# Performance work log

Hardware: AMD Instinct MI355X
Metric: run time of the kernel (lower is better)

Reference implementation:

```python
import jax, jax.numpy as jnp
import numpy as np

B, L, A, K = 8, 256, 15, 9
EDGE_SIZE = 16
CA = 1  # BBHeavyAtom.CA index


def setup_inputs() -> dict:
    key = jax.random.key(0)
    k1, k2, k3, k4 = jax.random.split(key, 4)
    pos_heavyatom = jax.random.normal(k1, (B, L, A, 3), jnp.float32) * 3.0
    aa = jax.random.randint(k2, (B, L), 0, 21, jnp.int32)
    atom_types = jax.random.randint(k3, (B, L, A), 0, 38, jnp.int32)
    mask_atoms = jnp.ones((B, L, A), dtype=bool)
    block_lengths = jnp.full((B, L), A, jnp.int32)
    lengths = jnp.full((B,), L, jnp.int32)
    # two segments per sample (e.g. antibody / antigen) so intra+inter edges exist
    fragment_type = jnp.broadcast_to((jnp.arange(L) >= L // 2).astype(jnp.int32), (B, L))
    edge_emb = jax.random.normal(k4, (2, EDGE_SIZE), jnp.float32) * 0.02
    return {"pos_heavyatom": pos_heavyatom, "aa": aa, "atom_types": atom_types,
            "mask_atoms": mask_atoms, "block_lengths": block_lengths,
            "lengths": lengths, "fragment_type": fragment_type, "edge_emb": edge_emb}


def _block_dist(pos, mask_atoms):
    """Min unit-pair distance between every pair of blocks. pos [B,L,A,3] -> [B,L,L]."""
    Xf = pos.reshape(B, L * A, 3)
    x2 = jnp.sum(Xf * Xf, axis=-1)  # [B, N]
    d2 = x2[:, :, None] + x2[:, None, :] - 2.0 * jnp.einsum('bnd,bmd->bnm', Xf, Xf)
    d = jnp.sqrt(jnp.maximum(d2, 0.0))  # [B, N, N]
    # unit is kept iff its atom mask AND its residue's CA mask are set
    mask_res = mask_atoms[:, :, CA]                           # [B, L]
    valid = (mask_atoms & mask_res[:, :, None]).reshape(B, L * A)
    pair_ok = valid[:, :, None] & valid[:, None, :]
    d = jnp.where(pair_ok, d, jnp.inf)
    # scatter_min over block edges == min over the (A, A) unit-pair tiles
    return d.reshape(B, L, A, L, A).min(axis=(2, 4))          # [B, L, L]


def _knn_edges(dist, cand_mask):
    """For each source block (row), pick K nearest candidate dst blocks. Returns [2, B*L*K] global ids."""
    dm = jnp.where(cand_mask, dist, jnp.inf)
    _, idx = jax.lax.top_k(-dm, K)                            # [B, L, K] local dst ids
    src = jnp.broadcast_to(jnp.arange(L, dtype=jnp.int32)[None, :, None], (B, L, K))
    offs = (jnp.arange(B, dtype=jnp.int32) * L)[:, None, None]
    return jnp.stack([(src + offs).reshape(-1), (idx.astype(jnp.int32) + offs).reshape(-1)], axis=0)


def reference(pos_heavyatom, aa, atom_types, mask_atoms, block_lengths, lengths,
              fragment_type, edge_emb):
    # segment ids: fragment_type 2 is merged into segment 1
    seg = jnp.where(fragment_type == 2, 1, fragment_type)     # [B, L]
    dist = _block_dist(pos_heavyatom, mask_atoms)             # [B, L, L]

    same_seg = seg[:, :, None] == seg[:, None, :]
    eye = jnp.eye(L, dtype=bool)[None]
    intra_edges = _knn_edges(dist, same_seg & ~eye)           # same segment, no self-loop
    inter_edges = _knn_edges(dist, ~same_seg)                 # different segment

    edges = jnp.concatenate([intra_edges, inter_edges], axis=1)  # [2, 2*B*L*K]
    edge_type = jnp.concatenate([jnp.zeros(intra_edges.shape[1], jnp.int32),
                                 jnp.ones(inter_edges.shape[1], jnp.int32)])
    edge_attr = edge_emb[edge_type]                           # [2*B*L*K, 16]

    block_id = jnp.arange(B * L * A, dtype=jnp.int32) // A    # global block id per unit
    batch_id = jnp.arange(B * L, dtype=jnp.int32) // L        # batch id per block
    return block_id, batch_id, edges, edge_attr
```

## Files before the change

### kernel.cpp

```cpp
#include <hip/hip_runtime.h>


#define BB   8
#define LL   256
#define AA   15
#define KK   9

#define O_EDGES   32768
#define NE_HALF   18432
#define NE        36864
#define O_ATTR    106496
#define N_ATTR    589824

__global__ __launch_bounds__(256) void dist_knn_kernel(
    const float* __restrict__ pos,
    const int*   __restrict__ frag,
    float*       __restrict__ out)
{
    const int b = blockIdx.x / LL;
    const int i = blockIdx.x % LL;
    const int j = threadIdx.x;

    __shared__ double dAi[AA * 3];
    __shared__ double dX2i[AA];
    __shared__ double sDist[LL];
    __shared__ int    sSeg[LL];

    if (j < AA * 3) dAi[j] = (double)pos[(size_t)(b * LL + i) * (AA * 3) + j];
    __syncthreads();
    if (j < AA) {
        double x0 = dAi[j * 3 + 0], x1 = dAi[j * 3 + 1], x2 = dAi[j * 3 + 2];
        dX2i[j] = x0 * x0 + x1 * x1 + x2 * x2;
    }

    double xj[AA][3];
    double x2j[AA];
    const float* pj = pos + (size_t)(b * LL + j) * (AA * 3);
    #pragma unroll
    for (int c = 0; c < AA; ++c) {
        xj[c][0] = (double)pj[c * 3 + 0];
        xj[c][1] = (double)pj[c * 3 + 1];
        xj[c][2] = (double)pj[c * 3 + 2];
        x2j[c] = xj[c][0] * xj[c][0] + xj[c][1] * xj[c][1] + xj[c][2] * xj[c][2];
    }
    int ft  = frag[b * LL + j];
    int seg = (ft == 2) ? 1 : ft;
    __syncthreads();

    double d2min = INFINITY;
    for (int a = 0; a < AA; ++a) {
        double a0 = dAi[a * 3 + 0], a1 = dAi[a * 3 + 1], a2 = dAi[a * 3 + 2];
        double x2a = dX2i[a];
        #pragma unroll
        for (int c = 0; c < AA; ++c) {
            double dot = a0 * xj[c][0] + a1 * xj[c][1] + a2 * xj[c][2];
            double d2  = (x2a + x2j[c]) - 2.0 * dot;
            d2min = fmin(d2min, d2);
        }
    }
    sDist[j] = fmax(d2min, 0.0);
    sSeg[j]  = seg;
    __syncthreads();

    if (j < 64) {
        const int seg_i = sSeg[i];
        const int row   = b * LL + i;
        for (int pass = 0; pass < 2; ++pass) {
            double dl[4];
            int    il[4];
            #pragma unroll
            for (int q = 0; q < 4; ++q) {
                int cand = j + q * 64;
                int sc   = sSeg[cand];
                bool ok  = (pass == 0) ? (sc == seg_i && cand != i)
                                       : (sc != seg_i);
                dl[q] = ok ? sDist[cand] : INFINITY;
                il[q] = cand;
            }
            for (int k = 0; k < KK; ++k) {
                double v = dl[0]; int id = il[0];
                #pragma unroll
                for (int q = 1; q < 4; ++q)
                    if (dl[q] < v || (dl[q] == v && il[q] < id)) { v = dl[q]; id = il[q]; }
                for (int off = 1; off < 64; off <<= 1) {
                    double ov = __shfl_xor(v, off, 64);
                    int    oi = __shfl_xor(id, off, 64);
                    if (ov < v || (ov == v && oi < id)) { v = ov; id = oi; }
                }
                if ((id & 63) == j) dl[id >> 6] = INFINITY;
                if (j == 0) {
                    int e = (pass == 0 ? 0 : NE_HALF) + row * KK + k;
                    out[O_EDGES + e]      = (float)row;
                    out[O_EDGES + NE + e] = (float)(b * LL + id);
                }
            }
        }
    }
}

__global__ __launch_bounds__(256) void fill_kernel(
    const float* __restrict__ emb,
    float*       __restrict__ out)
{
    __shared__ float semb[32];
    if (threadIdx.x < 32) semb[threadIdx.x] = emb[threadIdx.x];
    __syncthreads();

    int t = blockIdx.x * blockDim.x + threadIdx.x;
    if (t < 30720) out[t] = (float)(t / AA);
    if (t < 2048)  out[30720 + t] = (float)(t >> 8);
    if (t < N_ATTR) {
        int row = t >> 4;
        int col = t & 15;
        out[O_ATTR + t] = semb[(row < NE_HALF ? 0 : 16) + col];
    }
}

extern "C" void kernel_launch(void* const* d_in, const int* in_sizes, int n_in,
                              void* d_out, int out_size, void* d_ws, size_t ws_size,
                              hipStream_t stream) {
    const float* pos  = (const float*)d_in[0];
    const int*   frag = (const int*)d_in[6];
    const float* emb  = (const float*)d_in[7];
    float* out = (float*)d_out;

    dist_knn_kernel<<<dim3(BB * LL), dim3(256), 0, stream>>>(pos, frag, out);
    fill_kernel<<<dim3((N_ATTR + 255) / 256), dim3(256), 0, stream>>>(emb, out);
}
```

Before: 111.2 us.

## Screen distances in fp32, refine candidates in fp64, fuse fill kernel

The all-pairs min-distance pass now runs in fp32 with split min accumulators. Each row's 9th-nearest value per pass sets a threshold, and only candidates within a small margin of it have their distances recomputed in fp64. The final top-k selection then runs on those refined values, so ties and near-ties still resolve as before. The separate fill kernel for block_id, batch_id and edge_attr is folded into the same kernel, which removes a launch. The fixed DELTA margin risks missing a true neighbour if fp32 error exceeds it, and the refinement adds extra syncs and global reads.

```diff
diff --git a/kernel.cpp b/kernel.cpp
--- a/kernel.cpp
+++ b/kernel.cpp
@@ -6,75 +6,165 @@
 #define AA   15
 #define KK   9
 
+#define O_BATCH   30720
 #define O_EDGES   32768
 #define NE_HALF   18432
 #define NE        36864
 #define O_ATTR    106496
 #define N_ATTR    589824
-
-__global__ __launch_bounds__(256) void dist_knn_kernel(
+#define DELTA     0.02f
+
+__global__ __launch_bounds__(256) void edge_fused_kernel(
     const float* __restrict__ pos,
     const int*   __restrict__ frag,
+    const float* __restrict__ emb,
     float*       __restrict__ out)
 {
-    const int b = blockIdx.x / LL;
-    const int i = blockIdx.x % LL;
-    const int j = threadIdx.x;
-
-    __shared__ double dAi[AA * 3];
-    __shared__ double dX2i[AA];
-    __shared__ double sDist[LL];
+    const int blk = blockIdx.x;
+    const int b   = blk >> 8;
+    const int i   = blk & 255;
+    const int j   = threadIdx.x;
+
+    __shared__ float  sAi[45];
+    __shared__ float  sX2i[AA];
+    __shared__ float  sD32[LL];
     __shared__ int    sSeg[LL];
-
-    if (j < AA * 3) dAi[j] = (double)pos[(size_t)(b * LL + i) * (AA * 3) + j];
+    __shared__ double sD64[LL];
+    __shared__ int    sList[LL];
+    __shared__ int    sCnt;
+    __shared__ float  sV9[2];
+
+    if (j < AA)  out[blk * AA + j]  = (float)blk;
+    if (j == AA) out[O_BATCH + blk] = (float)b;
+    {
+        int idx = blk * 288 + j;
+        int e = idx >> 4, col = idx & 15;
+        out[O_ATTR + idx] = emb[(e < NE_HALF ? 0 : 16) + col];
+        if (j < 32) {
+            int idx2 = idx + 256;
+            int e2 = idx2 >> 4, col2 = idx2 & 15;
+            out[O_ATTR + idx2] = emb[(e2 < NE_HALF ? 0 : 16) + col2];
+        }
+    }
+
+    if (j < 45)  sAi[j] = pos[(size_t)blk * 45 + j];
+    if (j == 255) sCnt = 0;
+    sD64[j] = INFINITY;
     __syncthreads();
     if (j < AA) {
-        double x0 = dAi[j * 3 + 0], x1 = dAi[j * 3 + 1], x2 = dAi[j * 3 + 2];
-        dX2i[j] = x0 * x0 + x1 * x1 + x2 * x2;
-    }
-
-    double xj[AA][3];
-    double x2j[AA];
-    const float* pj = pos + (size_t)(b * LL + j) * (AA * 3);
+        float x0 = sAi[3*j], x1 = sAi[3*j+1], x2 = sAi[3*j+2];
+        sX2i[j] = x0*x0 + x1*x1 + x2*x2;
+    }
+
+    float xj[AA][3], x2j[AA];
+    const float* pj = pos + (size_t)(b * LL + j) * 45;
     #pragma unroll
     for (int c = 0; c < AA; ++c) {
-        xj[c][0] = (double)pj[c * 3 + 0];
-        xj[c][1] = (double)pj[c * 3 + 1];
-        xj[c][2] = (double)pj[c * 3 + 2];
-        x2j[c] = xj[c][0] * xj[c][0] + xj[c][1] * xj[c][1] + xj[c][2] * xj[c][2];
-    }
-    int ft  = frag[b * LL + j];
-    int seg = (ft == 2) ? 1 : ft;
-    __syncthreads();
-
-    double d2min = INFINITY;
+        xj[c][0] = pj[3*c]; xj[c][1] = pj[3*c+1]; xj[c][2] = pj[3*c+2];
+        x2j[c] = xj[c][0]*xj[c][0] + xj[c][1]*xj[c][1] + xj[c][2]*xj[c][2];
+    }
+    int ft = frag[b * LL + j];
+    sSeg[j] = (ft == 2) ? 1 : ft;
+    __syncthreads();
+
+    float m0 = INFINITY, m1 = INFINITY, m2 = INFINITY;
     for (int a = 0; a < AA; ++a) {
-        double a0 = dAi[a * 3 + 0], a1 = dAi[a * 3 + 1], a2 = dAi[a * 3 + 2];
-        double x2a = dX2i[a];
+        float a0 = sAi[3*a], a1 = sAi[3*a+1], a2 = sAi[3*a+2];
+        float x2a = sX2i[a];
         #pragma unroll
         for (int c = 0; c < AA; ++c) {
-            double dot = a0 * xj[c][0] + a1 * xj[c][1] + a2 * xj[c][2];
-            double d2  = (x2a + x2j[c]) - 2.0 * dot;
-            d2min = fmin(d2min, d2);
-        }
-    }
-    sDist[j] = fmax(d2min, 0.0);
-    sSeg[j]  = seg;
-    __syncthreads();
+            float dot = fmaf(a0, xj[c][0], fmaf(a1, xj[c][1], a2 * xj[c][2]));
+            float d2  = fmaf(-2.0f, dot, x2a + x2j[c]);
+            if      (c % 3 == 0) m0 = fminf(m0, d2);
+            else if (c % 3 == 1) m1 = fminf(m1, d2);
+            else                 m2 = fminf(m2, d2);
+        }
+    }
+    sD32[j] = fmaxf(fminf(m0, fminf(m1, m2)), 0.0f);
+    __syncthreads();
+
+    const int seg_i = sSeg[i];
 
     if (j < 64) {
-        const int seg_i = sSeg[i];
-        const int row   = b * LL + i;
         for (int pass = 0; pass < 2; ++pass) {
-            double dl[4];
-            int    il[4];
+            float dl[4]; int il[4];
             #pragma unroll
             for (int q = 0; q < 4; ++q) {
-                int cand = j + q * 64;
-                int sc   = sSeg[cand];
-                bool ok  = (pass == 0) ? (sc == seg_i && cand != i)
-                                       : (sc != seg_i);
-                dl[q] = ok ? sDist[cand] : INFINITY;
+                int cand = j + (q << 6);
+                bool ok = (pass == 0) ? (sSeg[cand] == seg_i && cand != i)
+                                      : (sSeg[cand] != seg_i);
+                dl[q] = ok ? sD32[cand] : INFINITY;
+                il[q] = cand;
+            }
+            float v9 = INFINITY;
+            for (int k = 0; k < KK; ++k) {
+                float v = dl[0]; int id = il[0];
+                #pragma unroll
+                for (int q = 1; q < 4; ++q)
+                    if (dl[q] < v || (dl[q] == v && il[q] < id)) { v = dl[q]; id = il[q]; }
+                for (int off = 1; off < 64; off <<= 1) {
+                    float ov = __shfl_xor(v, off, 64);
+                    int   oi = __shfl_xor(id, off, 64);
+                    if (ov < v || (ov == v && oi < id)) { v = ov; id = oi; }
+                }
+                if ((id & 63) == j) dl[id >> 6] = INFINITY;
+                v9 = v;
+            }
+            if (j == 0) sV9[pass] = v9;
+        }
+    }
+    __syncthreads();
+
+    {
+        bool okI = (sSeg[j] == seg_i) && (j != i);
+        bool okX = (sSeg[j] != seg_i);
+        float dj = sD32[j];
+        bool mark = (okI && dj <= sV9[0] + DELTA) ||
+                    (okX && dj <= sV9[1] + DELTA);
+        if (mark) { int p = atomicAdd(&sCnt, 1); sList[p] = j; }
+    }
+    __syncthreads();
+    const int cnt = sCnt;
+
+    {
+        const int wv = j >> 6, lane = j & 63;
+        for (int base = 0; base < cnt; base += 4) {
+            int k = base + wv;
+            double dmin = INFINITY;
+            int cand = 0;
+            if (k < cnt) {
+                cand = sList[k];
+                const float* pc = pos + (size_t)(b * LL + cand) * 45;
+                for (int p = lane; p < 225; p += 64) {
+                    int a = p / 15, c = p - a * 15;
+                    double ax = (double)sAi[3*a], ay = (double)sAi[3*a+1],
+                           az = (double)sAi[3*a+2];
+                    double cx = (double)pc[3*c], cy = (double)pc[3*c+1],
+                           cz = (double)pc[3*c+2];
+                    double dot = ax*cx + ay*cy + az*cz;
+                    double d2  = (ax*ax + ay*ay + az*az)
+                               + (cx*cx + cy*cy + cz*cz) - 2.0 * dot;
+                    dmin = fmin(dmin, d2);
+                }
+            }
+            #pragma unroll
+            for (int off = 1; off < 64; off <<= 1)
+                dmin = fmin(dmin, __shfl_xor(dmin, off, 64));
+            if (lane == 0 && k < cnt) sD64[cand] = fmax(dmin, 0.0);
+        }
+    }
+    __syncthreads();
+
+    if (j < 64) {
+        const int row = blk;
+        for (int pass = 0; pass < 2; ++pass) {
+            double dl[4]; int il[4];
+            #pragma unroll
+            for (int q = 0; q < 4; ++q) {
+                int cand = j + (q << 6);
+                bool ok = (pass == 0) ? (sSeg[cand] == seg_i && cand != i)
+                                      : (sSeg[cand] != seg_i);
+                dl[q] = ok ? sD64[cand] : INFINITY;
                 il[q] = cand;
             }
             for (int k = 0; k < KK; ++k) {
@@ -98,24 +188,6 @@
     }
 }
 
-__global__ __launch_bounds__(256) void fill_kernel(
-    const float* __restrict__ emb,
-    float*       __restrict__ out)
-{
-    __shared__ float semb[32];
-    if (threadIdx.x < 32) semb[threadIdx.x] = emb[threadIdx.x];
-    __syncthreads();
-
-    int t = blockIdx.x * blockDim.x + threadIdx.x;
-    if (t < 30720) out[t] = (float)(t / AA);
-    if (t < 2048)  out[30720 + t] = (float)(t >> 8);
-    if (t < N_ATTR) {
-        int row = t >> 4;
-        int col = t & 15;
-        out[O_ATTR + t] = semb[(row < NE_HALF ? 0 : 16) + col];
-    }
-}
-
 extern "C" void kernel_launch(void* const* d_in, const int* in_sizes, int n_in,
                               void* d_out, int out_size, void* d_ws, size_t ws_size,
                               hipStream_t stream) {
@@ -124,6 +196,5 @@
     const float* emb  = (const float*)d_in[7];
     float* out = (float*)d_out;
 
-    dist_knn_kernel<<<dim3(BB * LL), dim3(256), 0, stream>>>(pos, frag, out);
-    fill_kernel<<<dim3((N_ATTR + 255) / 256), dim3(256), 0, stream>>>(emb, out);
+    edge_fused_kernel<<<dim3(BB * LL), dim3(256), 0, stream>>>(pos, frag, emb, out);
 }
```

Result: slower. 132.1 us (+18.8%).
